# Kernel optimization log

Measured on AMD Instinct MI355X. Metric: run time of the kernel, lower is better.

The kernel has to match this reference:

```python
import jax, jax.numpy as jnp
import numpy as np

NUM_CROPS = 2
NUM_CLASSES = 1000
FEA_DIM = 1024
MOMENTUM = 0.9
B = 32768  # labels per batch; N = B * NUM_CROPS samples


def setup_inputs() -> dict:
    key = jax.random.key(0)
    k1, k2, k3, k4 = jax.random.split(key, 4)
    x = jax.random.normal(k1, (B * NUM_CROPS, FEA_DIM), dtype=jnp.float32)
    # centers start as unit-norm rows (as they would be after prior updates)
    ci = jax.random.normal(k2, (NUM_CLASSES, FEA_DIM), dtype=jnp.float32)
    ci = ci / jnp.linalg.norm(ci, axis=1, keepdims=True)
    cs = jax.random.normal(k3, (NUM_CLASSES, FEA_DIM), dtype=jnp.float32)
    cs = cs / jnp.linalg.norm(cs, axis=1, keepdims=True)
    l = jax.random.randint(k4, (B,), 0, NUM_CLASSES, dtype=jnp.int64)
    return {"x": x, "center_img": ci, "center_skt": cs, "l": l}


def reference(x, center_img, center_skt, l):
    # world_size = 1 -> all_gather is identity; labels tiled num_crops times
    all_l = jnp.tile(l, NUM_CROPS)  # [N]
    # per-class scatter-add (replaces the per-sample python loop)
    sums = jax.ops.segment_sum(x, all_l, num_segments=NUM_CLASSES)  # [C, D]
    counts = jax.ops.segment_sum(jnp.ones((all_l.shape[0],), x.dtype), all_l,
                                 num_segments=NUM_CLASSES)  # [C]
    present = counts > 0  # classes_in_batch mask
    center_tmp = sums / jnp.maximum(counts, 1.0)[:, None]  # per-class mean
    # momentum EMA + L2 normalize for classes present in batch (modality='img')
    upd = center_img * MOMENTUM + center_tmp * (1.0 - MOMENTUM)
    upd = upd / jnp.linalg.norm(upd, axis=1, keepdims=True)
    new_img = jnp.where(present[:, None], upd, center_img)
    # align_loss(center_img[cls], center_skt[cls], alpha=2) = mean ||diff||^2
    diff = new_img - center_skt
    per_cls = jnp.sum(diff * diff, axis=1)  # norm(p=2)^2
    n_present = jnp.sum(present.astype(x.dtype))
    loss = jnp.sum(jnp.where(present, per_cls, 0.0)) / n_present
    return loss  # * world_size (=1)
```

## Files before the change

### kernel.cpp

```cpp
#include <hip/hip_runtime.h>

#define NB    32768
#define NC    1000
#define ND    1024
#define ND4   256
#define MOM   0.9f


__global__ void hist_k(const int* __restrict__ l, int* __restrict__ counts) {
    int i = blockIdx.x * blockDim.x + threadIdx.x;
    if (i < NB) atomicAdd(&counts[l[i]], 1);
}

__global__ void scan_k(const int* __restrict__ counts, int* __restrict__ offsets) {
    __shared__ int s[1024];
    int t = threadIdx.x;
    int v = (t < NC) ? counts[t] : 0;
    s[t] = v;
    __syncthreads();
    for (int o = 1; o < 1024; o <<= 1) {
        int a = (t >= o) ? s[t - o] : 0;
        __syncthreads();
        s[t] += a;
        __syncthreads();
    }
    offsets[t] = s[t] - v;
}

__global__ void scatter_k(const int* __restrict__ l, const int* __restrict__ offsets,
                          int* __restrict__ cursors, int* __restrict__ sorted) {
    int i = blockIdx.x * blockDim.x + threadIdx.x;
    if (i < NB) {
        int c = l[i];
        int pos = offsets[c] + atomicAdd(&cursors[c], 1);
        sorted[pos] = i;
    }
}

__device__ __forceinline__ float block_sum(float v, float* sm, int t) {
    __syncthreads();
    #pragma unroll
    for (int o = 32; o > 0; o >>= 1) v += __shfl_down(v, o, 64);
    if ((t & 63) == 0) sm[t >> 6] = v;
    __syncthreads();
    if (t == 0) sm[0] = sm[0] + sm[1] + sm[2] + sm[3];
    __syncthreads();
    return sm[0];
}

__global__ __launch_bounds__(256) void class_k(
        const float4* __restrict__ x4,
        const float4* __restrict__ ci4,
        const float4* __restrict__ cs4,
        const int* __restrict__ counts,
        const int* __restrict__ offsets,
        const int* __restrict__ sorted,
        float* __restrict__ loss_acc) {
    int c = blockIdx.x;
    int t = threadIdx.x;
    int cnt = counts[c];
    int off = offsets[c];

    float4 acc = make_float4(0.f, 0.f, 0.f, 0.f);
    int j = 0;
    for (; j + 2 <= cnt; j += 2) {
        int i0 = sorted[off + j];
        int i1 = sorted[off + j + 1];
        float4 a0 = x4[(long)i0 * ND4 + t];
        float4 b0 = x4[((long)i0 + NB) * ND4 + t];
        float4 a1 = x4[(long)i1 * ND4 + t];
        float4 b1 = x4[((long)i1 + NB) * ND4 + t];
        acc.x += (a0.x + b0.x) + (a1.x + b1.x);
        acc.y += (a0.y + b0.y) + (a1.y + b1.y);
        acc.z += (a0.z + b0.z) + (a1.z + b1.z);
        acc.w += (a0.w + b0.w) + (a1.w + b1.w);
    }
    if (j < cnt) {
        int i0 = sorted[off + j];
        float4 a0 = x4[(long)i0 * ND4 + t];
        float4 b0 = x4[((long)i0 + NB) * ND4 + t];
        acc.x += a0.x + b0.x;
        acc.y += a0.y + b0.y;
        acc.z += a0.z + b0.z;
        acc.w += a0.w + b0.w;
    }

    float inv = 1.0f / fmaxf((float)cnt, 1.0f);
    float4 ci = ci4[c * ND4 + t];
    float4 upd;
    upd.x = ci.x * MOM + (acc.x * inv) * (1.0f - MOM);
    upd.y = ci.y * MOM + (acc.y * inv) * (1.0f - MOM);
    upd.z = ci.z * MOM + (acc.z * inv) * (1.0f - MOM);
    upd.w = ci.w * MOM + (acc.w * inv) * (1.0f - MOM);

    __shared__ float sm[4];
    float n2 = block_sum(upd.x * upd.x + upd.y * upd.y + upd.z * upd.z + upd.w * upd.w,
                         sm, t);
    float rn = 1.0f / sqrtf(n2);

    float4 nw;
    if (cnt > 0) {
        nw.x = upd.x * rn; nw.y = upd.y * rn; nw.z = upd.z * rn; nw.w = upd.w * rn;
    } else {
        nw = ci;
    }

    float4 cs = cs4[c * ND4 + t];
    float dx = nw.x - cs.x, dy = nw.y - cs.y, dz = nw.z - cs.z, dw = nw.w - cs.w;
    float lp = block_sum(dx * dx + dy * dy + dz * dz + dw * dw, sm, t);

    if (t == 0 && cnt > 0) {
        atomicAdd(&loss_acc[0], lp);
        atomicAdd(&loss_acc[1], 1.0f);
    }
}

__global__ void final_k(const float* __restrict__ loss_acc, float* __restrict__ out) {
    out[0] = loss_acc[0] / fmaxf(loss_acc[1], 1.0f);
}

extern "C" void kernel_launch(void* const* d_in, const int* in_sizes, int n_in,
                              void* d_out, int out_size, void* d_ws, size_t ws_size,
                              hipStream_t stream) {
    const float* x  = (const float*)d_in[0];
    const float* ci = (const float*)d_in[1];
    const float* cs = (const float*)d_in[2];
    const int*   l  = (const int*)d_in[3];
    float* out = (float*)d_out;

    int* ws      = (int*)d_ws;
    int* counts  = ws;
    int* cursors = ws + 1024;
    float* loss  = (float*)(ws + 2048);
    int* offsets = ws + 3072;
    int* sorted  = ws + 4096;

    hipMemsetAsync(d_ws, 0, 2050 * sizeof(int), stream);

    hist_k<<<NB / 256, 256, 0, stream>>>(l, counts);
    scan_k<<<1, 1024, 0, stream>>>(counts, offsets);
    scatter_k<<<NB / 256, 256, 0, stream>>>(l, offsets, cursors, sorted);
    class_k<<<NC, 256, 0, stream>>>((const float4*)x, (const float4*)ci,
                                    (const float4*)cs, counts, offsets, sorted, loss);
    final_k<<<1, 1, 0, stream>>>(loss, out);
}
```

Baseline: 400.9 us.

## Split per-class gather-sum across eight blocks with a partial-sum reduction stage

Adds a partial_k kernel that splits each class's sample gather across eight blocks, each summing a strided subset of that class's sorted rows into a workspace buffer. class_k then adds up the eight partials instead of walking all samples itself. The goal is to raise parallelism and memory-level concurrency beyond 1000 blocks, each doing a serial loop of about 33 sample pairs. The cost is one more kernel launch and about 32 MB of partial-sum traffic written and read back.

```diff
diff --git a/kernel.cpp b/kernel.cpp
--- a/kernel.cpp
+++ b/kernel.cpp
@@ -5,6 +5,7 @@
 #define ND    1024
 #define ND4   256
 #define MOM   0.9f
+#define SEG   8
 
 
 __global__ void hist_k(const int* __restrict__ l, int* __restrict__ counts) {
@@ -37,6 +38,31 @@
     }
 }
 
+__global__ __launch_bounds__(256) void partial_k(
+        const float4* __restrict__ x4,
+        const int* __restrict__ counts,
+        const int* __restrict__ offsets,
+        const int* __restrict__ sorted,
+        float4* __restrict__ part) {
+    int c = blockIdx.x >> 3;
+    int s = blockIdx.x & (SEG - 1);
+    int t = threadIdx.x;
+    int cnt = counts[c];
+    int off = offsets[c];
+
+    float4 acc = make_float4(0.f, 0.f, 0.f, 0.f);
+    for (int j = s; j < cnt; j += SEG) {
+        int i0 = sorted[off + j];
+        float4 a = x4[(long)i0 * ND4 + t];
+        float4 b = x4[((long)i0 + NB) * ND4 + t];
+        acc.x += a.x + b.x;
+        acc.y += a.y + b.y;
+        acc.z += a.z + b.z;
+        acc.w += a.w + b.w;
+    }
+    part[(long)blockIdx.x * ND4 + t] = acc;
+}
+
 __device__ __forceinline__ float block_sum(float v, float* sm, int t) {
     __syncthreads();
     #pragma unroll
@@ -49,40 +75,20 @@
 }
 
 __global__ __launch_bounds__(256) void class_k(
-        const float4* __restrict__ x4,
+        const float4* __restrict__ part,
         const float4* __restrict__ ci4,
         const float4* __restrict__ cs4,
         const int* __restrict__ counts,
-        const int* __restrict__ offsets,
-        const int* __restrict__ sorted,
         float* __restrict__ loss_acc) {
     int c = blockIdx.x;
     int t = threadIdx.x;
     int cnt = counts[c];
-    int off = offsets[c];
 
     float4 acc = make_float4(0.f, 0.f, 0.f, 0.f);
-    int j = 0;
-    for (; j + 2 <= cnt; j += 2) {
-        int i0 = sorted[off + j];
-        int i1 = sorted[off + j + 1];
-        float4 a0 = x4[(long)i0 * ND4 + t];
-        float4 b0 = x4[((long)i0 + NB) * ND4 + t];
-        float4 a1 = x4[(long)i1 * ND4 + t];
-        float4 b1 = x4[((long)i1 + NB) * ND4 + t];
-        acc.x += (a0.x + b0.x) + (a1.x + b1.x);
-        acc.y += (a0.y + b0.y) + (a1.y + b1.y);
-        acc.z += (a0.z + b0.z) + (a1.z + b1.z);
-        acc.w += (a0.w + b0.w) + (a1.w + b1.w);
-    }
-    if (j < cnt) {
-        int i0 = sorted[off + j];
-        float4 a0 = x4[(long)i0 * ND4 + t];
-        float4 b0 = x4[((long)i0 + NB) * ND4 + t];
-        acc.x += a0.x + b0.x;
-        acc.y += a0.y + b0.y;
-        acc.z += a0.z + b0.z;
-        acc.w += a0.w + b0.w;
+    #pragma unroll
+    for (int s = 0; s < SEG; ++s) {
+        float4 p = part[((long)c * SEG + s) * ND4 + t];
+        acc.x += p.x; acc.y += p.y; acc.z += p.z; acc.w += p.w;
     }
 
     float inv = 1.0f / fmaxf((float)cnt, 1.0f);
@@ -134,13 +140,16 @@
     float* loss  = (float*)(ws + 2048);
     int* offsets = ws + 3072;
     int* sorted  = ws + 4096;
+    float4* part = (float4*)(ws + 65536);
 
     hipMemsetAsync(d_ws, 0, 2050 * sizeof(int), stream);
 
     hist_k<<<NB / 256, 256, 0, stream>>>(l, counts);
     scan_k<<<1, 1024, 0, stream>>>(counts, offsets);
     scatter_k<<<NB / 256, 256, 0, stream>>>(l, offsets, cursors, sorted);
-    class_k<<<NC, 256, 0, stream>>>((const float4*)x, (const float4*)ci,
-                                    (const float4*)cs, counts, offsets, sorted, loss);
+    partial_k<<<NC * SEG, 256, 0, stream>>>((const float4*)x, counts, offsets,
+                                            sorted, part);
+    class_k<<<NC, 256, 0, stream>>>((const float4*)part, (const float4*)ci,
+                                    (const float4*)cs, counts, loss);
     final_k<<<1, 1, 0, stream>>>(loss, out);
 }
```

Result: slower. 426.8 us (+6.5%).
